# Optimization experiments

Hardware: AMD Instinct MI355X
Metric: run time of the kernel (lower is better)

The kernel has to match this reference:

```python
import jax, jax.numpy as jnp
import numpy as np

D = 512
H = 8
DK = D // H
EXP = 2
EPS = 1e-5


def _layernorm(x, g, b):
    mu = jnp.mean(x, axis=-1, keepdims=True)
    var = jnp.mean(jnp.square(x - mu), axis=-1, keepdims=True)
    return (x - mu) * jax.lax.rsqrt(var + EPS) * g + b


def setup_inputs() -> dict:
    key = jax.random.key(0)
    ks = jax.random.split(key, 10)
    B, C = 4, 2048
    s = 0.02
    return {
        "h": jax.random.normal(ks[0], (B, C, D), jnp.float32),
        "adj_bias": jax.random.normal(ks[1], (B, C, C), jnp.float32),
        "w_qkv": jax.random.normal(ks[2], (D, 3 * D), jnp.float32) * s,
        "b_qkv": jnp.zeros((3 * D,), jnp.float32),
        "w_out": jax.random.normal(ks[3], (D, D), jnp.float32) * s,
        "b_out": jnp.zeros((D,), jnp.float32),
        "ln1_g": jnp.ones((D,), jnp.float32),
        "ln1_b": jnp.zeros((D,), jnp.float32),
        "ln2_g": jnp.ones((D,), jnp.float32),
        "ln2_b": jnp.zeros((D,), jnp.float32),
        "w1": jax.random.normal(ks[4], (D, D * EXP), jnp.float32) * s,
        "b1": jnp.zeros((D * EXP,), jnp.float32),
        "w2": jax.random.normal(ks[5], (D * EXP, D), jnp.float32) * s,
        "b2": jnp.zeros((D,), jnp.float32),
    }


def reference(h, adj_bias, w_qkv, b_qkv, w_out, b_out, ln1_g, ln1_b, ln2_g, ln2_b, w1, b1, w2, b2):
    B, C, _ = h.shape
    scale = DK ** -0.5
    h_n = _layernorm(h, ln1_g, ln1_b)
    qkv = (h_n @ w_qkv + b_qkv).reshape(B, C, 3, H, DK)
    q, k, v = (qkv[:, :, i].transpose(0, 2, 1, 3) for i in range(3))  # (B,H,C,DK)
    logits = jnp.einsum('bhqd,bhkd->bhqk', q, k) * scale + adj_bias[:, None, :, :]
    attn = jax.nn.softmax(logits, axis=-1)  # (B,H,C,C); dropout off (eval)
    out = jnp.einsum('bhqk,bhkd->bhqd', attn, v).transpose(0, 2, 1, 3).reshape(B, C, D)
    h = h + out @ w_out + b_out
    ff = _layernorm(h, ln2_g, ln2_b)
    ff = jax.nn.gelu(ff @ w1 + b1, approximate=False) @ w2 + b2
    return h + ff
```

## Files before the change

kernel.cpp:

```cpp
#include <hip/hip_runtime.h>
#include <hip/hip_bf16.h>

#define BDIM 4
#define CDIM 2048
#define DDIM 512
#define HH   8
#define DKH  64
#define NROW (BDIM * CDIM)

typedef unsigned short u16;
typedef unsigned int   u32;
typedef u16   u16x4  __attribute__((ext_vector_type(4)));
typedef u16   u16x8  __attribute__((ext_vector_type(8)));
typedef u32   u32x4  __attribute__((ext_vector_type(4)));
typedef __bf16 bf16x8 __attribute__((ext_vector_type(8)));
typedef __bf16 bf16x2 __attribute__((ext_vector_type(2)));
typedef float f32x4  __attribute__((ext_vector_type(4)));
typedef float f32x16 __attribute__((ext_vector_type(16)));

#define LOG2E 1.4426950408889634f

__device__ __forceinline__ u16 f2bf(float f) {
  union { float f; unsigned u; } x; x.f = f;
  unsigned u = x.u;
  u += 0x7fffu + ((u >> 16) & 1u);
  return (u16)(u >> 16);
}
__device__ __forceinline__ float bf2f(u16 u) {
  return __builtin_bit_cast(float, (u32)u << 16);
}
__device__ __forceinline__ u32 pk2(float a, float b) {
  bf16x2 t; t[0] = (__bf16)a; t[1] = (__bf16)b;
  return __builtin_bit_cast(u32, t);
}
__device__ __forceinline__ float fexp2(float x) {
  float r;
  asm("v_exp_f32 %0, %1" : "=v"(r) : "v"(x));
  return r;
}

__device__ __forceinline__ void gload_lds16(const u16* gp, u16* lp) {
  __builtin_amdgcn_global_load_lds((__attribute__((address_space(1))) const void*)gp,
                                   (__attribute__((address_space(3))) void*)lp, 16, 0, 0);
}

__global__ __launch_bounds__(256) void ln_kernel(const float* __restrict__ x,
                                                 const float* __restrict__ gamma,
                                                 const float* __restrict__ beta,
                                                 u16* __restrict__ y, int nrows) {
  int gw = (blockIdx.x * 256 + threadIdx.x) >> 6;
  int l  = threadIdx.x & 63;
  if (gw >= nrows) return;
  const float* xr = x + (size_t)gw * DDIM;
  float4 a = *(const float4*)(xr + l * 8);
  float4 b = *(const float4*)(xr + l * 8 + 4);
  float s = a.x + a.y + a.z + a.w + b.x + b.y + b.z + b.w;
  float q = a.x*a.x + a.y*a.y + a.z*a.z + a.w*a.w + b.x*b.x + b.y*b.y + b.z*b.z + b.w*b.w;
#pragma unroll
  for (int m = 1; m < 64; m <<= 1) { s += __shfl_xor(s, m); q += __shfl_xor(q, m); }
  float mu  = s * (1.0f / DDIM);
  float var = q * (1.0f / DDIM) - mu * mu;
  float rs  = rsqrtf(var + 1e-5f);
  float4 g0 = *(const float4*)(gamma + l * 8);
  float4 g1 = *(const float4*)(gamma + l * 8 + 4);
  float4 b0 = *(const float4*)(beta + l * 8);
  float4 b1 = *(const float4*)(beta + l * 8 + 4);
  u16x8 o;
  o[0] = f2bf((a.x - mu) * rs * g0.x + b0.x);
  o[1] = f2bf((a.y - mu) * rs * g0.y + b0.y);
  o[2] = f2bf((a.z - mu) * rs * g0.z + b0.z);
  o[3] = f2bf((a.w - mu) * rs * g0.w + b0.w);
  o[4] = f2bf((b.x - mu) * rs * g1.x + b1.x);
  o[5] = f2bf((b.y - mu) * rs * g1.y + b1.y);
  o[6] = f2bf((b.z - mu) * rs * g1.z + b1.z);
  o[7] = f2bf((b.w - mu) * rs * g1.w + b1.w);
  *(u16x8*)(y + (size_t)gw * DDIM + l * 8) = o;
}

__global__ __launch_bounds__(256) void transpose_all(const float* __restrict__ wqkv,
                                                     const float* __restrict__ wout,
                                                     const float* __restrict__ w1,
                                                     const float* __restrict__ w2,
                                                     u16* __restrict__ o_qkv,
                                                     u16* __restrict__ o_out,
                                                     u16* __restrict__ o_w1,
                                                     u16* __restrict__ o_w2) {
  int idx = blockIdx.x * 256 + threadIdx.x;
  const float* w; u16* wt; int K, N;
  if (idx < 98304)       { w = wqkv; wt = o_qkv; K = 512;  N = 1536; }
  else if (idx < 131072) { idx -= 98304;  w = wout; wt = o_out; K = 512;  N = 512; }
  else if (idx < 196608) { idx -= 131072; w = w1;   wt = o_w1;  K = 512;  N = 1024; }
  else                   { idx -= 196608; w = w2;   wt = o_w2;  K = 1024; N = 512; }
  int kb = K >> 3;
  int n = idx / kb, k0 = (idx - n * kb) * 8;
  u16x8 o;
#pragma unroll
  for (int j = 0; j < 8; ++j) o[j] = f2bf(w[(size_t)(k0 + j) * N + n]);
  *(u16x8*)(wt + (size_t)n * K + k0) = o;
}

__global__ __launch_bounds__(256) void adj_transform(const float* __restrict__ adj,
                                                     u16* __restrict__ adjC) {
  const int bkt = blockIdx.y;
  const int b = bkt >> 5, kt = bkt & 31;
  const int q0 = blockIdx.x * 256;
  const int t = threadIdx.x;
  const int ch = t & 7, c16 = ch & 3, hi2 = ch >> 2, m = c16 >> 1;
  const int K0 = m * 32 + ((c16 * 2) & 3) * 8 + hi2 * 4;
#pragma unroll
  for (int itq = 0; itq < 8; ++itq) {
    int q = q0 + itq * 32 + (t >> 3);
    const float* src = adj + ((size_t)b * CDIM + q) * CDIM + kt * 64;
    f32x4 v0 = *(const f32x4*)(src + K0);
    f32x4 v1 = *(const f32x4*)(src + K0 + 8);
    u16x8 o;
    o[0] = f2bf(v0[0] * LOG2E); o[1] = f2bf(v0[1] * LOG2E);
    o[2] = f2bf(v0[2] * LOG2E); o[3] = f2bf(v0[3] * LOG2E);
    o[4] = f2bf(v1[0] * LOG2E); o[5] = f2bf(v1[1] * LOG2E);
    o[6] = f2bf(v1[2] * LOG2E); o[7] = f2bf(v1[3] * LOG2E);
    *(u16x8*)(adjC + ((size_t)(b * 32 + kt) * 2048 + q) * 64 + ch * 8) = o;
  }
}

template <int EPI>
__global__ __launch_bounds__(256) void gemm64(const u16* __restrict__ A,
                                              const u16* __restrict__ Bt,
                                              const float* __restrict__ bias,
                                              const float* __restrict__ res,
                                              float* __restrict__ outf,
                                              u16* __restrict__ outb,
                                              u16* __restrict__ outq,
                                              u16* __restrict__ outk,
                                              u16* __restrict__ outv,
                                              int M, int N, int K) {
  __shared__ u16 As[2][64 * 32];
  __shared__ u16 Bs[2][128 * 32];
  const int tid = threadIdx.x;
  const int w = tid >> 6, l = tid & 63;
  const int l15 = l & 15, l4 = l >> 4;
  const int bm = blockIdx.y, bn = blockIdx.x;

  f32x4 acc[4][2] = {};

  const u16* Ag = A  + (size_t)(bm * 64 + w * 16 + (l >> 2)) * K + (l & 3) * 8;
  const u16* Bg = Bt + (size_t)(bn * 128 + w * 32 + (l >> 2)) * K + (l & 3) * 8;

  auto stage = [&](int buf, int k0) {
    gload_lds16(Ag + k0, &As[buf][w * 512]);
    gload_lds16(Bg + k0, &Bs[buf][w * 1024]);
    gload_lds16(Bg + (size_t)16 * K + k0, &Bs[buf][w * 1024 + 512]);
  };

  stage(0, 0);
  __syncthreads();
  int cur = 0;
  for (int k0 = 0; k0 < K; k0 += 32) {
    if (k0 + 32 < K) stage(cur ^ 1, k0 + 32);
    bf16x8 af[4], bf[2];
#pragma unroll
    for (int m = 0; m < 4; ++m)
      af[m] = *(const bf16x8*)(&As[cur][(m * 16 + l15) * 32 + l4 * 8]);
#pragma unroll
    for (int n = 0; n < 2; ++n)
      bf[n] = *(const bf16x8*)(&Bs[cur][(w * 32 + n * 16 + l15) * 32 + l4 * 8]);
#pragma unroll
    for (int m = 0; m < 4; ++m)
#pragma unroll
      for (int n = 0; n < 2; ++n)
        acc[m][n] = __builtin_amdgcn_mfma_f32_16x16x32_bf16(af[m], bf[n], acc[m][n], 0, 0, 0);
    __syncthreads();
    cur ^= 1;
  }

#pragma unroll
  for (int m = 0; m < 4; ++m) {
    const int row0 = bm * 64 + m * 16 + l4 * 4;
#pragma unroll
    for (int n = 0; n < 2; ++n) {
      const int col = bn * 128 + w * 32 + n * 16 + l15;
      const float bv = bias[col];
#pragma unroll
      for (int r = 0; r < 4; ++r) {
        const int row = row0 + r;
        float val = acc[m][n][r] + bv;
        if constexpr (EPI == 0) {
          int t = col >> 9, hh = (col >> 6) & 7, dk = col & 63;
          int bb = row >> 11, cc = row & 2047;
          if (t == 0) {
            val *= 0.125f * LOG2E;
            outq[(((size_t)bb * HH + hh) * CDIM + cc) * DKH + dk] = f2bf(val);
          } else if (t == 1) {
            outk[(((size_t)bb * HH + hh) * CDIM + cc) * DKH + dk] = f2bf(val);
          } else {
            outv[(((size_t)bb * HH + hh) * DKH + dk) * CDIM + cc] = f2bf(val);
          }
        } else if constexpr (EPI == 1) {
          size_t idx = (size_t)row * N + col;
          outf[idx] = val + res[idx];
        } else {
          float g = 0.5f * val * (1.0f + erff(val * 0.70710678118f));
          outb[(size_t)row * N + col] = f2bf(g);
        }
      }
    }
  }
}

__global__ __launch_bounds__(512, 2) void flash_attn(const u16* __restrict__ Q,
                                                     const u16* __restrict__ Kg,
                                                     const u16* __restrict__ Vt,
                                                     const u16* __restrict__ adjC,
                                                     u16* __restrict__ O) {
  __shared__ u16 Ks[2][2][64 * 64];
  __shared__ u16 Vs[2][2][64 * 64];
  __shared__ float lw[4][32];
  __shared__ float lsx[4][32];
  const int flat = blockIdx.x + 16 * blockIdx.y;
  const int virt = (flat & 7) * 64 + (flat >> 3);
  const int qt = virt & 15;
  const int bh = virt >> 4;
  const int b = bh >> 3, hh = bh & 7;
  const int tid = threadIdx.x;
  const int w = tid >> 6, l = tid & 63;
  const int kh = w >> 2, qg = w & 3;
  const int q32 = l & 31, hi = l >> 5;
  const int qglob = qt * 128 + qg * 32 + q32;

  const u16* Qb = Q  + (size_t)bh * CDIM * DKH;
  const u16* Kb = Kg + (size_t)bh * CDIM * DKH;
  const u16* Vb = Vt + (size_t)bh * DKH * CDIM;

  const int srow = qg * 16 + (l >> 3);
  const int sg   = (l & 7) ^ (l >> 3);
  const u16* Kg0 = Kb + (size_t)(srow + 0) * DKH + sg * 8;
  const u16* Kg1 = Kb + (size_t)(srow + 8) * DKH + sg * 8;
  const u16* Vg0 = Vb + (size_t)(srow + 0) * CDIM + sg * 8;
  const u16* Vg1 = Vb + (size_t)(srow + 8) * CDIM + sg * 8;

  bf16x8 qf[4];
#pragma unroll
  for (int s = 0; s < 4; ++s)
    qf[s] = *(const bf16x8*)(Qb + (size_t)qglob * DKH + s * 16 + hi * 8);

  const u16* adjQ = adjC + ((size_t)(b * 32) * 2048 + qglob) * 64 + hi * 32;

  f32x16 oa[2] = {};
  float lsum = 0.f;

  auto stage = [&](int buf, int ktr) {
    int kta = kh * 16 + ktr;
    gload_lds16(Kg0 + (size_t)kta * 4096, &Ks[kh][buf][(qg * 16 + 0) * 64]);
    gload_lds16(Kg1 + (size_t)kta * 4096, &Ks[kh][buf][(qg * 16 + 8) * 64]);
    gload_lds16(Vg0 + kta * 64, &Vs[kh][buf][(qg * 16 + 0) * 64]);
    gload_lds16(Vg1 + kta * 64, &Vs[kh][buf][(qg * 16 + 8) * 64]);
  };
  auto ajload = [&](u16x8* dst, int ktr) {
    const u16* p = adjQ + (size_t)(kh * 16 + ktr) * 131072;
#pragma unroll
    for (int i = 0; i < 4; ++i) dst[i] = *(const u16x8*)(p + i * 8);
  };
  auto computeQK = [&](const u16* KsB, const u16x8* av, f32x16* sa) {
#pragma unroll
    for (int m = 0; m < 2; ++m)
#pragma unroll
      for (int r = 0; r < 16; ++r)
        sa[m][r] = bf2f(av[m * 2 + (r >> 3)][r & 7]);
    __builtin_amdgcn_s_setprio(1);
#pragma unroll
    for (int s = 0; s < 4; ++s)
#pragma unroll
      for (int m = 0; m < 2; ++m) {
        bf16x8 kf = *(const bf16x8*)(&KsB[(m * 32 + q32) * 64 + (((s * 2 + hi) ^ (q32 & 7)) * 8)]);
        sa[m] = __builtin_amdgcn_mfma_f32_32x32x16_bf16(kf, qf[s], sa[m], 0, 0, 0);
      }
    __builtin_amdgcn_s_setprio(0);
  };
  auto computePV = [&](const u16* VsB, f32x16* sa) {
#pragma unroll
    for (int m = 0; m < 2; ++m)
#pragma unroll
      for (int r = 0; r < 16; ++r) {
        float p = fexp2(sa[m][r]);
        sa[m][r] = p;
        lsum += p;
      }
    bf16x8 af[4];
#pragma unroll
    for (int m = 0; m < 2; ++m)
#pragma unroll
      for (int t2 = 0; t2 < 2; ++t2) {
        u32 w0 = pk2(sa[m][t2 * 8 + 0], sa[m][t2 * 8 + 1]);
        u32 w1 = pk2(sa[m][t2 * 8 + 2], sa[m][t2 * 8 + 3]);
        u32 w2 = pk2(sa[m][t2 * 8 + 4], sa[m][t2 * 8 + 5]);
        u32 w3 = pk2(sa[m][t2 * 8 + 6], sa[m][t2 * 8 + 7]);
        auto r02 = __builtin_amdgcn_permlane32_swap(w0, w2, false, false);
        auto r13 = __builtin_amdgcn_permlane32_swap(w1, w3, false, false);
        u32x4 aw;
        aw[0] = r02[0];
        aw[1] = r13[0];
        aw[2] = r02[1];
        aw[3] = r13[1];
        af[m * 2 + t2] = __builtin_bit_cast(bf16x8, aw);
      }
    __builtin_amdgcn_s_setprio(1);
#pragma unroll
    for (int s = 0; s < 4; ++s)
#pragma unroll
      for (int n = 0; n < 2; ++n) {
        bf16x8 vf = *(const bf16x8*)(&VsB[(n * 32 + q32) * 64 + (((s * 2 + hi) ^ (q32 & 7)) * 8)]);
        oa[n] = __builtin_amdgcn_mfma_f32_32x32x16_bf16(af[s], vf, oa[n], 0, 0, 0);
      }
    __builtin_amdgcn_s_setprio(0);
  };

  u16x8 avA[4], avB[4];
  f32x16 sa[2];
  stage(0, 0);
  ajload(avA, 0);
  __syncthreads();
#pragma unroll 1
  for (int it = 0; it < 8; ++it) {
    int ktr = it * 2;
    stage(1, ktr + 1);
    computeQK(&Ks[kh][0][0], avA, sa);
    ajload(avB, ktr + 1);
    computePV(&Vs[kh][0][0], sa);
    __syncthreads();
    if (ktr + 2 < 16) stage(0, ktr + 2);
    computeQK(&Ks[kh][1][0], avB, sa);
    if (ktr + 2 < 16) ajload(avA, ktr + 2);
    computePV(&Vs[kh][1][0], sa);
    __syncthreads();
  }

  lsum += __shfl_xor(lsum, 32);

  float* cb = (float*)&Vs[0][0][0];
  if (kh == 1) {
#pragma unroll
    for (int n = 0; n < 2; ++n)
#pragma unroll
      for (int r = 0; r < 16; ++r)
        cb[((qg * 2 + n) * 16 + r) * 64 + l] = oa[n][r];
    if (hi == 0) lsx[qg][q32] = lsum;
  }
  __syncthreads();
  if (kh == 0) {
    lsum += lsx[qg][q32];
#pragma unroll
    for (int n = 0; n < 2; ++n)
#pragma unroll
      for (int r = 0; r < 16; ++r)
        oa[n][r] += cb[((qg * 2 + n) * 16 + r) * 64 + l];
    lw[qg][q32] = 1.0f / lsum;
#pragma unroll
    for (int n = 0; n < 2; ++n)
#pragma unroll
      for (int r = 0; r < 16; ++r) {
        int qloc = (r & 3) + 8 * (r >> 2) + 4 * hi;
        int row = qt * 128 + qg * 32 + qloc;
        float val = oa[n][r] * lw[qg][qloc];
        O[((size_t)b * CDIM + row) * DDIM + hh * 64 + n * 32 + q32] = f2bf(val);
      }
  }
}

extern "C" void kernel_launch(void* const* d_in, const int* in_sizes, int n_in,
                              void* d_out, int out_size, void* d_ws, size_t ws_size,
                              hipStream_t stream) {
  const float* h      = (const float*)d_in[0];
  const float* adj    = (const float*)d_in[1];
  const float* w_qkv  = (const float*)d_in[2];
  const float* b_qkv  = (const float*)d_in[3];
  const float* w_out  = (const float*)d_in[4];
  const float* b_out  = (const float*)d_in[5];
  const float* ln1g   = (const float*)d_in[6];
  const float* ln1b   = (const float*)d_in[7];
  const float* ln2g   = (const float*)d_in[8];
  const float* ln2b   = (const float*)d_in[9];
  const float* w1     = (const float*)d_in[10];
  const float* b1     = (const float*)d_in[11];
  const float* w2     = (const float*)d_in[12];
  const float* b2     = (const float*)d_in[13];
  float* out = (float*)d_out;

  char* ws = (char*)d_ws;
  u16* adjC  = (u16*)(ws);
  u16* hn    = (u16*)(ws + 33554432);
  u16* qb    = (u16*)(ws + 41943040);
  u16* kb    = (u16*)(ws + 50331648);
  u16* vt    = (u16*)(ws + 58720256);
  u16* attn  = (u16*)(ws + 67108864);
  u16* wqkvt = (u16*)(ws + 75497472);
  u16* woutt = (u16*)(ws + 77070336);
  u16* w1t   = (u16*)(ws + 77594624);
  u16* w2t   = (u16*)(ws + 78643200);
  u16* ffin  = hn;
  u16* ffmid = qb;

  adj_transform<<<dim3(8, 128), 256, 0, stream>>>(adj, adjC);

  transpose_all<<<1024, 256, 0, stream>>>(w_qkv, w_out, w1, w2,
                                          wqkvt, woutt, w1t, w2t);

  ln_kernel<<<2048, 256, 0, stream>>>(h, ln1g, ln1b, hn, NROW);

  gemm64<0><<<dim3(12, 128), 256, 0, stream>>>(hn, wqkvt, b_qkv, nullptr,
                                               nullptr, nullptr, qb, kb, vt,
                                               NROW, 3 * DDIM, DDIM);

  flash_attn<<<dim3(16, 32), 512, 0, stream>>>(qb, kb, vt, adjC, attn);

  gemm64<1><<<dim3(4, 128), 256, 0, stream>>>(attn, woutt, b_out, h,
                                              out, nullptr, nullptr, nullptr, nullptr,
                                              NROW, DDIM, DDIM);

  ln_kernel<<<2048, 256, 0, stream>>>(out, ln2g, ln2b, ffin, NROW);

  gemm64<2><<<dim3(8, 128), 256, 0, stream>>>(ffin, w1t, b1, nullptr,
                                              nullptr, ffmid, nullptr, nullptr, nullptr,
                                              NROW, 2 * DDIM, DDIM);

  gemm64<1><<<dim3(4, 128), 256, 0, stream>>>(ffmid, w2t, b2, out,
                                              out, nullptr, nullptr, nullptr, nullptr,
                                              NROW, DDIM, 2 * DDIM);
}
```

Measured before the change: 197.1 us.

## Use triple-buffered LDS in GEMM and deeper prefetch with explicit vmcnt waits in attention

```diff
diff --git a/kernel.cpp b/kernel.cpp
--- a/kernel.cpp
+++ b/kernel.cpp
@@ -19,6 +19,12 @@
 typedef float f32x16 __attribute__((ext_vector_type(16)));
 
 #define LOG2E 1.4426950408889634f
+
+#define MEMFENCE asm volatile("" ::: "memory")
+__device__ __forceinline__ void sbar() {
+  MEMFENCE; __builtin_amdgcn_s_barrier(); MEMFENCE;
+}
+#define VMWAIT(N) asm volatile("s_waitcnt vmcnt(" #N ")" ::: "memory")
 
 __device__ __forceinline__ u16 f2bf(float f) {
   union { float f; unsigned u; } x; x.f = f;
@@ -133,8 +139,8 @@
                                               u16* __restrict__ outk,
                                               u16* __restrict__ outv,
                                               int M, int N, int K) {
-  __shared__ u16 As[2][64 * 32];
-  __shared__ u16 Bs[2][128 * 32];
+  __shared__ u16 As[3][64 * 32];
+  __shared__ u16 Bs[3][128 * 32];
   const int tid = threadIdx.x;
   const int w = tid >> 6, l = tid & 63;
   const int l15 = l & 15, l4 = l >> 4;
@@ -151,25 +157,32 @@
     gload_lds16(Bg + (size_t)16 * K + k0, &Bs[buf][w * 1024 + 512]);
   };
 
+  const int nk = K >> 5;
   stage(0, 0);
-  __syncthreads();
-  int cur = 0;
-  for (int k0 = 0; k0 < K; k0 += 32) {
-    if (k0 + 32 < K) stage(cur ^ 1, k0 + 32);
+  stage(1, 32);
+  VMWAIT(3); sbar();
+#pragma unroll 1
+  for (int i = 0; i < nk; ++i) {
+    const u16* AsC = &As[i % 3][0];
+    const u16* BsC = &Bs[i % 3][0];
     bf16x8 af[4], bf[2];
 #pragma unroll
     for (int m = 0; m < 4; ++m)
-      af[m] = *(const bf16x8*)(&As[cur][(m * 16 + l15) * 32 + l4 * 8]);
+      af[m] = *(const bf16x8*)(&AsC[(m * 16 + l15) * 32 + l4 * 8]);
 #pragma unroll
     for (int n = 0; n < 2; ++n)
-      bf[n] = *(const bf16x8*)(&Bs[cur][(w * 32 + n * 16 + l15) * 32 + l4 * 8]);
+      bf[n] = *(const bf16x8*)(&BsC[(w * 32 + n * 16 + l15) * 32 + l4 * 8]);
 #pragma unroll
     for (int m = 0; m < 4; ++m)
 #pragma unroll
       for (int n = 0; n < 2; ++n)
         acc[m][n] = __builtin_amdgcn_mfma_f32_16x16x32_bf16(af[m], bf[n], acc[m][n], 0, 0, 0);
-    __syncthreads();
-    cur ^= 1;
+    if (i + 1 < nk) {
+      sbar();
+      if (i + 2 < nk) { stage((i + 2) % 3, (i + 2) * 32); VMWAIT(3); }
+      else            { VMWAIT(0); }
+      sbar();
+    }
   }
 
 #pragma unroll
@@ -316,22 +329,32 @@
   u16x8 avA[4], avB[4];
   f32x16 sa[2];
   stage(0, 0);
+  stage(1, 1);
   ajload(avA, 0);
-  __syncthreads();
+  VMWAIT(4); sbar();
 #pragma unroll 1
-  for (int it = 0; it < 8; ++it) {
-    int ktr = it * 2;
-    stage(1, ktr + 1);
+  for (int it2 = 0; it2 < 7; ++it2) {
+    int ktr = it2 * 2;
     computeQK(&Ks[kh][0][0], avA, sa);
     ajload(avB, ktr + 1);
     computePV(&Vs[kh][0][0], sa);
-    __syncthreads();
-    if (ktr + 2 < 16) stage(0, ktr + 2);
+    sbar();
+    stage(0, ktr + 2);
+    VMWAIT(4); sbar();
     computeQK(&Ks[kh][1][0], avB, sa);
-    if (ktr + 2 < 16) ajload(avA, ktr + 2);
+    ajload(avA, ktr + 2);
     computePV(&Vs[kh][1][0], sa);
-    __syncthreads();
-  }
+    sbar();
+    stage(1, ktr + 3);
+    VMWAIT(4); sbar();
+  }
+  computeQK(&Ks[kh][0][0], avA, sa);
+  ajload(avB, 15);
+  computePV(&Vs[kh][0][0], sa);
+  VMWAIT(0); sbar();
+  computeQK(&Ks[kh][1][0], avB, sa);
+  computePV(&Vs[kh][1][0], sa);
+  __syncthreads();
 
   lsum += __shfl_xor(lsum, 32);
 
```

Measured after the change: 204.7 us. 3.8% more time.

## Merge setup kernels into one launch and widen GEMM K-tile with swizzled LDS

Applied to the files above, without the earlier changes.

```diff
diff --git a/kernel.cpp b/kernel.cpp
--- a/kernel.cpp
+++ b/kernel.cpp
@@ -44,13 +44,13 @@
                                    (__attribute__((address_space(3))) void*)lp, 16, 0, 0);
 }
 
-__global__ __launch_bounds__(256) void ln_kernel(const float* __restrict__ x,
-                                                 const float* __restrict__ gamma,
-                                                 const float* __restrict__ beta,
-                                                 u16* __restrict__ y, int nrows) {
-  int gw = (blockIdx.x * 256 + threadIdx.x) >> 6;
-  int l  = threadIdx.x & 63;
-  if (gw >= nrows) return;
+__device__ __forceinline__ void ln_body(int bx, int tid,
+                                        const float* __restrict__ x,
+                                        const float* __restrict__ gamma,
+                                        const float* __restrict__ beta,
+                                        u16* __restrict__ y) {
+  int gw = (bx * 256 + tid) >> 6;
+  int l  = tid & 63;
   const float* xr = x + (size_t)gw * DDIM;
   float4 a = *(const float4*)(xr + l * 8);
   float4 b = *(const float4*)(xr + l * 8 + 4);
@@ -77,48 +77,63 @@
   *(u16x8*)(y + (size_t)gw * DDIM + l * 8) = o;
 }
 
-__global__ __launch_bounds__(256) void transpose_all(const float* __restrict__ wqkv,
-                                                     const float* __restrict__ wout,
-                                                     const float* __restrict__ w1,
-                                                     const float* __restrict__ w2,
-                                                     u16* __restrict__ o_qkv,
-                                                     u16* __restrict__ o_out,
-                                                     u16* __restrict__ o_w1,
-                                                     u16* __restrict__ o_w2) {
-  int idx = blockIdx.x * 256 + threadIdx.x;
-  const float* w; u16* wt; int K, N;
-  if (idx < 98304)       { w = wqkv; wt = o_qkv; K = 512;  N = 1536; }
-  else if (idx < 131072) { idx -= 98304;  w = wout; wt = o_out; K = 512;  N = 512; }
-  else if (idx < 196608) { idx -= 131072; w = w1;   wt = o_w1;  K = 512;  N = 1024; }
-  else                   { idx -= 196608; w = w2;   wt = o_w2;  K = 1024; N = 512; }
-  int kb = K >> 3;
-  int n = idx / kb, k0 = (idx - n * kb) * 8;
-  u16x8 o;
-#pragma unroll
-  for (int j = 0; j < 8; ++j) o[j] = f2bf(w[(size_t)(k0 + j) * N + n]);
-  *(u16x8*)(wt + (size_t)n * K + k0) = o;
-}
-
-__global__ __launch_bounds__(256) void adj_transform(const float* __restrict__ adj,
-                                                     u16* __restrict__ adjC) {
-  const int bkt = blockIdx.y;
-  const int b = bkt >> 5, kt = bkt & 31;
-  const int q0 = blockIdx.x * 256;
+__global__ __launch_bounds__(256) void ln_kernel(const float* __restrict__ x,
+                                                 const float* __restrict__ gamma,
+                                                 const float* __restrict__ beta,
+                                                 u16* __restrict__ y) {
+  ln_body(blockIdx.x, threadIdx.x, x, gamma, beta, y);
+}
+
+__global__ __launch_bounds__(256) void setup_kernel(const float* __restrict__ h,
+                                                    const float* __restrict__ ln1g,
+                                                    const float* __restrict__ ln1b,
+                                                    u16* __restrict__ hn,
+                                                    const float* __restrict__ adj,
+                                                    u16* __restrict__ adjC,
+                                                    const float* __restrict__ wqkv,
+                                                    const float* __restrict__ wout,
+                                                    const float* __restrict__ w1,
+                                                    const float* __restrict__ w2,
+                                                    u16* __restrict__ o_qkv,
+                                                    u16* __restrict__ o_out,
+                                                    u16* __restrict__ o_w1,
+                                                    u16* __restrict__ o_w2) {
+  const int bx = blockIdx.x;
   const int t = threadIdx.x;
-  const int ch = t & 7, c16 = ch & 3, hi2 = ch >> 2, m = c16 >> 1;
-  const int K0 = m * 32 + ((c16 * 2) & 3) * 8 + hi2 * 4;
-#pragma unroll
-  for (int itq = 0; itq < 8; ++itq) {
-    int q = q0 + itq * 32 + (t >> 3);
-    const float* src = adj + ((size_t)b * CDIM + q) * CDIM + kt * 64;
-    f32x4 v0 = *(const f32x4*)(src + K0);
-    f32x4 v1 = *(const f32x4*)(src + K0 + 8);
+  if (bx < 2048) {
+    ln_body(bx, t, h, ln1g, ln1b, hn);
+  } else if (bx < 3072) {
+    const int f = bx - 2048;
+    const int b = f >> 8, kt = (f >> 3) & 31;
+    const int q0 = (f & 7) * 256;
+    const int ch = t & 7, c16 = ch & 3, hi2 = ch >> 2, m = c16 >> 1;
+    const int K0 = m * 32 + ((c16 * 2) & 3) * 8 + hi2 * 4;
+#pragma unroll
+    for (int itq = 0; itq < 8; ++itq) {
+      int q = q0 + itq * 32 + (t >> 3);
+      const float* src = adj + ((size_t)b * CDIM + q) * CDIM + kt * 64;
+      f32x4 v0 = *(const f32x4*)(src + K0);
+      f32x4 v1 = *(const f32x4*)(src + K0 + 8);
+      u16x8 o;
+      o[0] = f2bf(v0[0] * LOG2E); o[1] = f2bf(v0[1] * LOG2E);
+      o[2] = f2bf(v0[2] * LOG2E); o[3] = f2bf(v0[3] * LOG2E);
+      o[4] = f2bf(v1[0] * LOG2E); o[5] = f2bf(v1[1] * LOG2E);
+      o[6] = f2bf(v1[2] * LOG2E); o[7] = f2bf(v1[3] * LOG2E);
+      *(u16x8*)(adjC + ((size_t)(b * 32 + kt) * 2048 + q) * 64 + ch * 8) = o;
+    }
+  } else {
+    int idx = (bx - 3072) * 256 + t;
+    const float* w; u16* wt; int K, N;
+    if (idx < 98304)       { w = wqkv; wt = o_qkv; K = 512;  N = 1536; }
+    else if (idx < 131072) { idx -= 98304;  w = wout; wt = o_out; K = 512;  N = 512; }
+    else if (idx < 196608) { idx -= 131072; w = w1;   wt = o_w1;  K = 512;  N = 1024; }
+    else                   { idx -= 196608; w = w2;   wt = o_w2;  K = 1024; N = 512; }
+    int kb = K >> 3;
+    int n = idx / kb, k0 = (idx - n * kb) * 8;
     u16x8 o;
-    o[0] = f2bf(v0[0] * LOG2E); o[1] = f2bf(v0[1] * LOG2E);
-    o[2] = f2bf(v0[2] * LOG2E); o[3] = f2bf(v0[3] * LOG2E);
-    o[4] = f2bf(v1[0] * LOG2E); o[5] = f2bf(v1[1] * LOG2E);
-    o[6] = f2bf(v1[2] * LOG2E); o[7] = f2bf(v1[3] * LOG2E);
-    *(u16x8*)(adjC + ((size_t)(b * 32 + kt) * 2048 + q) * 64 + ch * 8) = o;
+#pragma unroll
+    for (int j = 0; j < 8; ++j) o[j] = f2bf(w[(size_t)(k0 + j) * N + n]);
+    *(u16x8*)(wt + (size_t)n * K + k0) = o;
   }
 }
 
@@ -133,41 +148,48 @@
                                               u16* __restrict__ outk,
                                               u16* __restrict__ outv,
                                               int M, int N, int K) {
-  __shared__ u16 As[2][64 * 32];
-  __shared__ u16 Bs[2][128 * 32];
+  __shared__ u16 As[2][64 * 64];
+  __shared__ u16 Bs[2][128 * 64];
   const int tid = threadIdx.x;
   const int w = tid >> 6, l = tid & 63;
-  const int l15 = l & 15, l4 = l >> 4;
+  const int l15 = l & 15, l4 = l >> 4, l7 = l15 & 7;
   const int bm = blockIdx.y, bn = blockIdx.x;
 
   f32x4 acc[4][2] = {};
 
-  const u16* Ag = A  + (size_t)(bm * 64 + w * 16 + (l >> 2)) * K + (l & 3) * 8;
-  const u16* Bg = Bt + (size_t)(bn * 128 + w * 32 + (l >> 2)) * K + (l & 3) * 8;
+  const int sg = (l & 7) ^ (l >> 3);
+  const u16* Ag = A  + (size_t)(bm * 64  + w * 16 + (l >> 3)) * K + sg * 8;
+  const u16* Bg = Bt + (size_t)(bn * 128 + w * 32 + (l >> 3)) * K + sg * 8;
 
   auto stage = [&](int buf, int k0) {
-    gload_lds16(Ag + k0, &As[buf][w * 512]);
-    gload_lds16(Bg + k0, &Bs[buf][w * 1024]);
-    gload_lds16(Bg + (size_t)16 * K + k0, &Bs[buf][w * 1024 + 512]);
+    gload_lds16(Ag + k0,                  &As[buf][(w * 16 + 0) * 64]);
+    gload_lds16(Ag + (size_t)8 * K + k0,  &As[buf][(w * 16 + 8) * 64]);
+    gload_lds16(Bg + k0,                  &Bs[buf][(w * 32 + 0) * 64]);
+    gload_lds16(Bg + (size_t)8 * K + k0,  &Bs[buf][(w * 32 + 8) * 64]);
+    gload_lds16(Bg + (size_t)16 * K + k0, &Bs[buf][(w * 32 + 16) * 64]);
+    gload_lds16(Bg + (size_t)24 * K + k0, &Bs[buf][(w * 32 + 24) * 64]);
   };
 
   stage(0, 0);
   __syncthreads();
   int cur = 0;
-  for (int k0 = 0; k0 < K; k0 += 32) {
-    if (k0 + 32 < K) stage(cur ^ 1, k0 + 32);
-    bf16x8 af[4], bf[2];
-#pragma unroll
-    for (int m = 0; m < 4; ++m)
-      af[m] = *(const bf16x8*)(&As[cur][(m * 16 + l15) * 32 + l4 * 8]);
-#pragma unroll
-    for (int n = 0; n < 2; ++n)
-      bf[n] = *(const bf16x8*)(&Bs[cur][(w * 32 + n * 16 + l15) * 32 + l4 * 8]);
-#pragma unroll
-    for (int m = 0; m < 4; ++m)
+  for (int k0 = 0; k0 < K; k0 += 64) {
+    if (k0 + 64 < K) stage(cur ^ 1, k0 + 64);
+#pragma unroll
+    for (int s = 0; s < 2; ++s) {
+      bf16x8 af[4], bf[2];
+#pragma unroll
+      for (int m = 0; m < 4; ++m)
+        af[m] = *(const bf16x8*)(&As[cur][(m * 16 + l15) * 64 + (((s * 4 + l4) ^ l7) * 8)]);
 #pragma unroll
       for (int n = 0; n < 2; ++n)
-        acc[m][n] = __builtin_amdgcn_mfma_f32_16x16x32_bf16(af[m], bf[n], acc[m][n], 0, 0, 0);
+        bf[n] = *(const bf16x8*)(&Bs[cur][(w * 32 + n * 16 + l15) * 64 + (((s * 4 + l4) ^ l7) * 8)]);
+#pragma unroll
+      for (int m = 0; m < 4; ++m)
+#pragma unroll
+        for (int n = 0; n < 2; ++n)
+          acc[m][n] = __builtin_amdgcn_mfma_f32_16x16x32_bf16(af[m], bf[n], acc[m][n], 0, 0, 0);
+    }
     __syncthreads();
     cur ^= 1;
   }
@@ -398,12 +420,9 @@
   u16* ffin  = hn;
   u16* ffmid = qb;
 
-  adj_transform<<<dim3(8, 128), 256, 0, stream>>>(adj, adjC);
-
-  transpose_all<<<1024, 256, 0, stream>>>(w_qkv, w_out, w1, w2,
-                                          wqkvt, woutt, w1t, w2t);
-
-  ln_kernel<<<2048, 256, 0, stream>>>(h, ln1g, ln1b, hn, NROW);
+  setup_kernel<<<4096, 256, 0, stream>>>(h, ln1g, ln1b, hn, adj, adjC,
+                                         w_qkv, w_out, w1, w2,
+                                         wqkvt, woutt, w1t, w2t);
 
   gemm64<0><<<dim3(12, 128), 256, 0, stream>>>(hn, wqkvt, b_qkv, nullptr,
                                                nullptr, nullptr, qb, kb, vt,
@@ -415,7 +434,7 @@
                                               out, nullptr, nullptr, nullptr, nullptr,
                                               NROW, DDIM, DDIM);
 
-  ln_kernel<<<2048, 256, 0, stream>>>(out, ln2g, ln2b, ffin, NROW);
+  ln_kernel<<<2048, 256, 0, stream>>>(out, ln2g, ln2b, ffin);
 
   gemm64<2><<<dim3(8, 128), 256, 0, stream>>>(ffin, w1t, b1, nullptr,
                                               nullptr, ffmid, nullptr, nullptr, nullptr,
```

Result: faster. 191.3 us (-3.0%).
